# Performance work log

Hardware: AMD Instinct MI355X
Metric: run time of the kernel (lower is better)

Reference implementation:

```python
import jax, jax.numpy as jnp
import numpy as np

B, DIM_Z, N_SAMPLES = 256, 64, 32
LOG_2PI = float(np.log(2.0 * np.pi))
VAR_EPS = 0.0001


def log_pdf(mean, logvar, zs):
    # elementwise Gaussian log-density (per dim), matching torch log_pdf
    return -0.5 * LOG_2PI - 0.5 * logvar - (zs - mean) ** 2 / (2.0 * jnp.exp(logvar) + VAR_EPS)


def setup_inputs() -> dict:
    key = jax.random.key(0)
    k1, k2, k3, k4, k5 = jax.random.split(key, 5)
    return {
        "prior_mean": jax.random.normal(k1, (B, DIM_Z), dtype=jnp.float32),
        "prior_logvar": jax.random.normal(k2, (B, DIM_Z), dtype=jnp.float32),
        "post_mean": jax.random.normal(k3, (B, DIM_Z), dtype=jnp.float32),
        "post_logvar": jax.random.normal(k4, (B, DIM_Z), dtype=jnp.float32),
        "eps": jax.random.normal(k5, (B, DIM_Z, N_SAMPLES), dtype=jnp.float32),
    }


def reference(prior_mean, prior_logvar, post_mean, post_logvar, eps):
    batch_size = post_mean.shape[0]
    # reparameterized samples from each posterior: [B, D, S]
    zs = post_mean[:, :, None] + eps * jnp.exp(0.5 * post_logvar)[:, :, None]
    # log p_prior_j(z_{j,d,s}): [B, D, S]
    logp_priors_zs = log_pdf(prior_mean[:, :, None], prior_logvar[:, :, None], zs)
    # log p_post_i(z_{j,d,s}): [B(i), B(j), D, S] -- the big broadcast intermediate
    logp_posts_zs = log_pdf(post_mean[:, None, :, None], post_logvar[:, None, :, None], zs[None])
    # max-stabilized log-mean-exp over posteriors i == logsumexp - log(B)
    logp_agg_post_zs = jax.scipy.special.logsumexp(logp_posts_zs, axis=0) - jnp.log(
        jnp.asarray(batch_size, dtype=logp_posts_zs.dtype)
    )  # [B(j), D, S]
    density_gaps = logp_agg_post_zs - logp_priors_zs  # [B, D, S]
    kl = density_gaps.mean(axis=0)  # [D, S]
    kl = kl.sum(axis=0).mean(axis=-1)  # scalar
    return kl
```

## Files before the change

kernel.cpp:

```cpp
#include <hip/hip_runtime.h>
#include <math.h>

#define BATCH 256
#define DIMZ  64
#define NSAMP 32
#define JB    32

__global__ __launch_bounds__(256) void lpo_kl_kernel(
    const float* __restrict__ prior_mean,
    const float* __restrict__ prior_logvar,
    const float* __restrict__ post_mean,
    const float* __restrict__ post_logvar,
    const float* __restrict__ eps,
    float* __restrict__ out)
{
    constexpr float LOG_2PI = 1.8378770664093453f;
    constexpr float VAR_EPS = 1e-4f;
    constexpr float LOG2E   = 1.4426950408889634f;
    constexpr float LN2     = 0.6931471805599453f;
    constexpr float LOG_B   = 5.545177444479562f;

    __shared__ __align__(16) float A_s[BATCH];
    __shared__ __align__(16) float B_s[BATCH];
    __shared__ __align__(16) float C_s[BATCH];
    __shared__ float m_s[BATCH];
    __shared__ float sg_s[BATCH];
    __shared__ float wred[4];

    const int tid = threadIdx.x;
    const int d   = blockIdx.x & (DIMZ - 1);
    const int j0  = (blockIdx.x >> 6) * JB;

    {
        const int i   = tid;
        float m   = post_mean[i * DIMZ + d];
        float lv  = post_logvar[i * DIMZ + d];
        float den = 2.0f * __expf(lv) + VAR_EPS;
        float C   = LOG2E / den;
        float B   = 2.0f * m * C;
        float A   = LOG2E * (-0.5f * LOG_2PI - 0.5f * lv) - m * m * C;
        A_s[i]  = A;
        B_s[i]  = B;
        C_s[i]  = C;
        m_s[i]  = m;
        sg_s[i] = __expf(0.5f * lv);
    }
    __syncthreads();

    const int s  = tid & (NSAMP - 1);
    const int jj = tid >> 5;

    float z[4], nz2[4];
    #pragma unroll
    for (int k = 0; k < 4; ++k) {
        const int j = j0 + jj + 8 * k;
        z[k]   = m_s[j] + eps[(j * DIMZ + d) * NSAMP + s] * sg_s[j];
        nz2[k] = -(z[k] * z[k]);
    }

    float acc[4][4] = {};
    #pragma unroll 2
    for (int i = 0; i < BATCH; i += 4) {
        const float4 Av = *(const float4*)(A_s + i);
        const float4 Bv = *(const float4*)(B_s + i);
        const float4 Cv = *(const float4*)(C_s + i);
        #pragma unroll
        for (int k = 0; k < 4; ++k) {
            acc[0][k] += __builtin_amdgcn_exp2f(
                __builtin_fmaf(Cv.x, nz2[k], __builtin_fmaf(Bv.x, z[k], Av.x)));
            acc[1][k] += __builtin_amdgcn_exp2f(
                __builtin_fmaf(Cv.y, nz2[k], __builtin_fmaf(Bv.y, z[k], Av.y)));
            acc[2][k] += __builtin_amdgcn_exp2f(
                __builtin_fmaf(Cv.z, nz2[k], __builtin_fmaf(Bv.z, z[k], Av.z)));
            acc[3][k] += __builtin_amdgcn_exp2f(
                __builtin_fmaf(Cv.w, nz2[k], __builtin_fmaf(Bv.w, z[k], Av.w)));
        }
    }

    float contrib = 0.0f;
    #pragma unroll
    for (int k = 0; k < 4; ++k) {
        const int j = j0 + jj + 8 * k;
        const float sum = (acc[0][k] + acc[1][k]) + (acc[2][k] + acc[3][k]);
        const float lse_nat = LN2 * __builtin_amdgcn_logf(sum) - LOG_B;

        const float pm   = prior_mean[j * DIMZ + d];
        const float plv  = prior_logvar[j * DIMZ + d];
        const float pden = 2.0f * __expf(plv) + VAR_EPS;
        const float dz   = z[k] - pm;
        const float logp_prior = -0.5f * LOG_2PI - 0.5f * plv - dz * dz / pden;

        contrib += lse_nat - logp_prior;
    }
    contrib *= 1.0f / (BATCH * NSAMP);

    for (int off = 32; off > 0; off >>= 1)
        contrib += __shfl_down(contrib, off);
    if ((tid & 63) == 0) wred[tid >> 6] = contrib;
    __syncthreads();
    if (tid == 0)
        atomicAdd(out, (wred[0] + wred[1]) + (wred[2] + wred[3]));
}

extern "C" void kernel_launch(void* const* d_in, const int* in_sizes, int n_in,
                              void* d_out, int out_size, void* d_ws, size_t ws_size,
                              hipStream_t stream) {
    const float* prior_mean   = (const float*)d_in[0];
    const float* prior_logvar = (const float*)d_in[1];
    const float* post_mean    = (const float*)d_in[2];
    const float* post_logvar  = (const float*)d_in[3];
    const float* eps          = (const float*)d_in[4];
    float* out = (float*)d_out;

    hipMemsetAsync(out, 0, sizeof(float), stream);

    lpo_kl_kernel<<<dim3((BATCH / JB) * DIMZ), dim3(256), 0, stream>>>(
        prior_mean, prior_logvar, post_mean, post_logvar, eps, out);
}
```

Before: 86.54 us.

## Precompute per-dimension quadratic coefficient tables in a separate kernel, read via global loads

Moves the A/B/C coefficient computation for each posterior into a small pre-kernel that writes per-dimension tables to workspace. Each main block then reads these tables directly from global memory (uniform addresses, likely scalar or cached loads) instead of rebuilding them in LDS with a barrier, which removes redundant recomputation across the 8 j-blocks per dimension. It adds an extra kernel launch, a workspace round-trip, and global or cache loads in the inner loop in place of LDS reads. The unroll factor is also raised from 2 to 4.

Result: no change. 86.62 us (+0.1%).

```diff
diff --git a/kernel.cpp b/kernel.cpp
--- a/kernel.cpp
+++ b/kernel.cpp
@@ -6,64 +6,76 @@
 #define NSAMP 32
 #define JB    32
 
+__global__ __launch_bounds__(256) void lpo_tbl_kernel(
+    const float* __restrict__ post_mean,
+    const float* __restrict__ post_logvar,
+    float* __restrict__ tblA,
+    float* __restrict__ tblB,
+    float* __restrict__ tblC)
+{
+    constexpr float LOG_2PI = 1.8378770664093453f;
+    constexpr float VAR_EPS = 1e-4f;
+    constexpr float LOG2E   = 1.4426950408889634f;
+
+    const int d = blockIdx.x;
+    const int i = threadIdx.x;
+
+    const float m   = post_mean[i * DIMZ + d];
+    const float lv  = post_logvar[i * DIMZ + d];
+    const float den = 2.0f * __expf(lv) + VAR_EPS;
+    const float C   = LOG2E / den;
+    const float B   = 2.0f * m * C;
+    const float A   = LOG2E * (-0.5f * LOG_2PI - 0.5f * lv) - m * m * C;
+
+    tblA[d * BATCH + i] = A;
+    tblB[d * BATCH + i] = B;
+    tblC[d * BATCH + i] = C;
+}
+
 __global__ __launch_bounds__(256) void lpo_kl_kernel(
     const float* __restrict__ prior_mean,
     const float* __restrict__ prior_logvar,
     const float* __restrict__ post_mean,
     const float* __restrict__ post_logvar,
     const float* __restrict__ eps,
+    const float* __restrict__ tblA,
+    const float* __restrict__ tblB,
+    const float* __restrict__ tblC,
     float* __restrict__ out)
 {
     constexpr float LOG_2PI = 1.8378770664093453f;
     constexpr float VAR_EPS = 1e-4f;
-    constexpr float LOG2E   = 1.4426950408889634f;
     constexpr float LN2     = 0.6931471805599453f;
     constexpr float LOG_B   = 5.545177444479562f;
 
-    __shared__ __align__(16) float A_s[BATCH];
-    __shared__ __align__(16) float B_s[BATCH];
-    __shared__ __align__(16) float C_s[BATCH];
-    __shared__ float m_s[BATCH];
-    __shared__ float sg_s[BATCH];
     __shared__ float wred[4];
 
     const int tid = threadIdx.x;
     const int d   = blockIdx.x & (DIMZ - 1);
     const int j0  = (blockIdx.x >> 6) * JB;
-
-    {
-        const int i   = tid;
-        float m   = post_mean[i * DIMZ + d];
-        float lv  = post_logvar[i * DIMZ + d];
-        float den = 2.0f * __expf(lv) + VAR_EPS;
-        float C   = LOG2E / den;
-        float B   = 2.0f * m * C;
-        float A   = LOG2E * (-0.5f * LOG_2PI - 0.5f * lv) - m * m * C;
-        A_s[i]  = A;
-        B_s[i]  = B;
-        C_s[i]  = C;
-        m_s[i]  = m;
-        sg_s[i] = __expf(0.5f * lv);
-    }
-    __syncthreads();
-
-    const int s  = tid & (NSAMP - 1);
-    const int jj = tid >> 5;
+    const int s   = tid & (NSAMP - 1);
+    const int jj  = tid >> 5;
 
     float z[4], nz2[4];
     #pragma unroll
     for (int k = 0; k < 4; ++k) {
-        const int j = j0 + jj + 8 * k;
-        z[k]   = m_s[j] + eps[(j * DIMZ + d) * NSAMP + s] * sg_s[j];
+        const int j  = j0 + jj + 8 * k;
+        const float m  = post_mean[j * DIMZ + d];
+        const float lv = post_logvar[j * DIMZ + d];
+        z[k]   = m + eps[(j * DIMZ + d) * NSAMP + s] * __expf(0.5f * lv);
         nz2[k] = -(z[k] * z[k]);
     }
 
+    const float* __restrict__ Ap = tblA + d * BATCH;
+    const float* __restrict__ Bp = tblB + d * BATCH;
+    const float* __restrict__ Cp = tblC + d * BATCH;
+
     float acc[4][4] = {};
-    #pragma unroll 2
+    #pragma unroll 4
     for (int i = 0; i < BATCH; i += 4) {
-        const float4 Av = *(const float4*)(A_s + i);
-        const float4 Bv = *(const float4*)(B_s + i);
-        const float4 Cv = *(const float4*)(C_s + i);
+        const float4 Av = *(const float4*)(Ap + i);
+        const float4 Bv = *(const float4*)(Bp + i);
+        const float4 Cv = *(const float4*)(Cp + i);
         #pragma unroll
         for (int k = 0; k < 4; ++k) {
             acc[0][k] += __builtin_amdgcn_exp2f(
@@ -112,8 +124,16 @@
     const float* eps          = (const float*)d_in[4];
     float* out = (float*)d_out;
 
+    float* tblA = (float*)d_ws;
+    float* tblB = tblA + DIMZ * BATCH;
+    float* tblC = tblB + DIMZ * BATCH;
+
+    lpo_tbl_kernel<<<dim3(DIMZ), dim3(BATCH), 0, stream>>>(
+        post_mean, post_logvar, tblA, tblB, tblC);
+
     hipMemsetAsync(out, 0, sizeof(float), stream);
 
     lpo_kl_kernel<<<dim3((BATCH / JB) * DIMZ), dim3(256), 0, stream>>>(
-        prior_mean, prior_logvar, post_mean, post_logvar, eps, out);
+        prior_mean, prior_logvar, post_mean, post_logvar, eps,
+        tblA, tblB, tblC, out);
 }
```
